# Kernel optimization log

Hardware: AMD Instinct MI355X
Metric: run time of the kernel (lower is better)

Reference implementation:

```python
import jax, jax.numpy as jnp
import numpy as np

N, E, F_IN, HID, H, EDIM, G = 50000, 800000, 64, 32, 4, 4, 1024
NEG = 0.2  # LeakyReLU slope (GATv2Conv default)


def _glorot(key, shape):
    s = jnp.sqrt(6.0 / (shape[0] + shape[-1]))
    return jax.random.uniform(key, shape, minval=-s, maxval=s, dtype=jnp.float32)


def setup_inputs() -> dict:
    key = jax.random.key(0)
    ks = jax.random.split(key, 20)
    d = {}
    d["x"] = jax.random.normal(ks[0], (N, F_IN), dtype=jnp.float32)
    d["edge_index"] = jax.random.randint(ks[1], (2, E), 0, N)
    d["edge_attr"] = jax.random.normal(ks[2], (E, EDIM), dtype=jnp.float32)
    d["batch"] = jnp.sort(jax.random.randint(ks[3], (N,), 0, G))
    dims = [F_IN, HID * H, HID * H]
    i = 4
    for l, din in enumerate(dims, 1):
        d[f"Wl{l}"] = _glorot(ks[i], (din, H * HID)); i += 1
        d[f"bl{l}"] = jnp.zeros((H * HID,), jnp.float32)
        d[f"Wr{l}"] = _glorot(ks[i], (din, H * HID)); i += 1
        d[f"br{l}"] = jnp.zeros((H * HID,), jnp.float32)
        d[f"We{l}"] = _glorot(ks[i], (EDIM, H * HID)); i += 1
        d[f"att{l}"] = _glorot(ks[i], (H, HID)); i += 1
        d[f"bias{l}"] = jnp.zeros((H * HID,), jnp.float32)
    d["Wlin"] = _glorot(ks[i], (H * HID, 1)); i += 1
    d["blin"] = jnp.zeros((1,), jnp.float32)
    return d


def _add_self_loops(edge_index, edge_attr):
    # PyG add_self_loops with fill_value='mean': self-loop edge feature is the
    # mean of incoming-edge features (zeros for isolated targets).
    src0, dst0 = edge_index[0], edge_index[1]
    cnt = jax.ops.segment_sum(jnp.ones((src0.shape[0],), jnp.float32), dst0, num_segments=N)
    loop_attr = jax.ops.segment_sum(edge_attr, dst0, num_segments=N) / jnp.maximum(cnt, 1.0)[:, None]
    ar = jnp.arange(N)
    src = jnp.concatenate([src0, ar])
    dst = jnp.concatenate([dst0, ar])
    ea = jnp.concatenate([edge_attr, loop_attr], axis=0)
    return src, dst, ea


def _gatv2_conv(x, src, dst, ea, Wl, bl, Wr, br, We, att, bias):
    n = x.shape[0]
    xl = (x @ Wl + bl).reshape(n, H, HID)   # source transform (message values)
    xr = (x @ Wr + br).reshape(n, H, HID)   # target transform
    e = jax.nn.leaky_relu(xl[src] + xr[dst] + (ea @ We).reshape(-1, H, HID), NEG)  # [Etot,H,C]
    logit = jnp.einsum('ehc,hc->eh', e, att)
    # segment softmax over destination node (every node has a self-loop)
    m = jax.ops.segment_max(logit, dst, num_segments=n)
    p = jnp.exp(logit - m[dst])
    s = jax.ops.segment_sum(p, dst, num_segments=n)
    alpha = p / (s[dst] + 1e-16)
    out = jax.ops.segment_sum(alpha[:, :, None] * xl[src], dst, num_segments=n)
    return out.reshape(n, H * HID) + bias


def reference(x, edge_index, edge_attr, batch,
              Wl1, bl1, Wr1, br1, We1, att1, bias1,
              Wl2, bl2, Wr2, br2, We2, att2, bias2,
              Wl3, bl3, Wr3, br3, We3, att3, bias3,
              Wlin, blin):
    src, dst, ea = _add_self_loops(edge_index, edge_attr)
    h = jax.nn.relu(_gatv2_conv(x, src, dst, ea, Wl1, bl1, Wr1, br1, We1, att1, bias1))
    h = jax.nn.relu(_gatv2_conv(h, src, dst, ea, Wl2, bl2, Wr2, br2, We2, att2, bias2))
    h = _gatv2_conv(h, src, dst, ea, Wl3, bl3, Wr3, br3, We3, att3, bias3)
    # global mean pool over graphs
    cnt = jax.ops.segment_sum(jnp.ones((N,), jnp.float32), batch, num_segments=G)
    pooled = jax.ops.segment_sum(h, batch, num_segments=G) / jnp.maximum(cnt, 1.0)[:, None]
    # dropout p=0.35 is identity in eval mode
    return pooled @ Wlin + blin
```

## Files before the change

kernel.cpp:

```cpp
#include <hip/hip_runtime.h>
#include <math.h>

#define NN 50000
#define EE 800000
#define FIN 64
#define GG 1024
#define ETOT (EE + NN)
#define PSLOT 16

typedef float v2f __attribute__((ext_vector_type(2)));

__global__ __launch_bounds__(256) void k_init(int* __restrict__ deg, int* __restrict__ fillpos,
    float* __restrict__ psum, int* __restrict__ pcnt) {
  int i = blockIdx.x * 256 + threadIdx.x;
  if (i < NN) { deg[i] = 0; fillpos[i] = 0; }
  if (i < GG * PSLOT) { psum[i] = 0.f; pcnt[i] = 0; }
}

__global__ __launch_bounds__(256) void k_deg(const int* __restrict__ dst, int* __restrict__ deg,
    const int* __restrict__ batch, int* __restrict__ pcnt) {
  int e = blockIdx.x * 256 + threadIdx.x;
  if (e < NN) atomicAdd(&pcnt[(batch[e] << 4) | (e & (PSLOT - 1))], 1);
  if (e >= EE) return;
  atomicAdd(&deg[dst[e]], 1);
}

__global__ __launch_bounds__(256) void k_scan1(const int* __restrict__ deg, int* __restrict__ part) {
  __shared__ int s[256];
  int i = blockIdx.x * 256 + threadIdx.x;
  s[threadIdx.x] = (i < NN) ? deg[i] + 1 : 0;
  __syncthreads();
  for (int st = 128; st > 0; st >>= 1) {
    if (threadIdx.x < st) s[threadIdx.x] += s[threadIdx.x + st];
    __syncthreads();
  }
  if (threadIdx.x == 0) part[blockIdx.x] = s[0];
}

__global__ __launch_bounds__(256) void k_scan2(int* __restrict__ part, int nb, int* __restrict__ offsets) {
  __shared__ int s[256];
  int t = threadIdx.x;
  s[t] = (t < nb) ? part[t] : 0;
  __syncthreads();
  for (int st = 1; st < 256; st <<= 1) {
    int a = (t >= st) ? s[t - st] : 0;
    __syncthreads();
    s[t] += a;
    __syncthreads();
  }
  if (t < nb) part[t] = t ? s[t - 1] : 0;
  if (t == 0) offsets[NN] = ETOT;
}

__global__ __launch_bounds__(256) void k_scan3(const int* __restrict__ deg,
    const int* __restrict__ part, int* __restrict__ offsets) {
  __shared__ int s[256];
  int t = threadIdx.x;
  int i = blockIdx.x * 256 + t;
  int v = (i < NN) ? deg[i] + 1 : 0;
  s[t] = v;
  __syncthreads();
  for (int st = 1; st < 256; st <<= 1) {
    int a = (t >= st) ? s[t - st] : 0;
    __syncthreads();
    s[t] += a;
    __syncthreads();
  }
  if (i < NN) offsets[i] = part[blockIdx.x] + s[t] - v;
}

__global__ __launch_bounds__(256) void k_fill(const int* __restrict__ src,
    const int* __restrict__ dst, const int* __restrict__ offsets,
    const int* __restrict__ deg, int* __restrict__ fillpos,
    int2* __restrict__ pr) {
  int i = blockIdx.x * 256 + threadIdx.x;
  if (i < EE) {
    int d = dst[i];
    int p = offsets[d] + atomicAdd(&fillpos[d], 1);
    pr[p] = make_int2(i, src[i]);
  } else if (i < EE + NN) {
    int n = i - EE;
    int p = offsets[n] + deg[n];
    pr[p] = make_int2(EE + n, n);
  }
}

__global__ __launch_bounds__(256) void k_sort(const int* __restrict__ offsets,
    const int* __restrict__ deg, int2* __restrict__ pr) {
  int n = blockIdx.x * 256 + threadIdx.x;
  if (n >= NN) return;
  int lo = offsets[n], d = deg[n];
  for (int i = lo + 1; i < lo + d; i++) {
    int2 key = pr[i];
    int j = i - 1;
    while (j >= lo && pr[j].x > key.x) {
      pr[j + 1] = pr[j];
      j--;
    }
    pr[j + 1] = key;
  }
}

__global__ __launch_bounds__(256) void k_gather(const int2* __restrict__ pr,
    const float* __restrict__ edge_attr, float4* __restrict__ csr_ea) {
  int p = blockIdx.x * 256 + threadIdx.x;
  if (p >= ETOT) return;
  int eid = pr[p].x;
  if (eid < EE) csr_ea[p] = *(const float4*)(edge_attr + (size_t)eid * 4);
}

__global__ __launch_bounds__(256) void k_selfattr(const int* __restrict__ offsets,
    float4* __restrict__ csr_ea) {
  int wave = threadIdx.x >> 6, lane = threadIdx.x & 63;
  int n = blockIdx.x * 4 + wave;
  if (n >= NN) return;
  int lo = offsets[n], d = offsets[n + 1] - lo - 1;
  float4 s = make_float4(0.f, 0.f, 0.f, 0.f);
  for (int i = lane; i < d; i += 64) {
    float4 v = csr_ea[lo + i];
    s.x += v.x; s.y += v.y; s.z += v.z; s.w += v.w;
  }
  #pragma unroll
  for (int off = 1; off < 64; off <<= 1) {
    s.x += __shfl_xor(s.x, off);
    s.y += __shfl_xor(s.y, off);
    s.z += __shfl_xor(s.z, off);
    s.w += __shfl_xor(s.w, off);
  }
  if (lane == 0) {
    float inv = 1.f / fmaxf((float)d, 1.f);
    csr_ea[lo + d] = make_float4(s.x * inv, s.y * inv, s.z * inv, s.w * inv);
  }
}

__global__ __launch_bounds__(256) void k_gemm(const float* __restrict__ X, int K,
    const float* __restrict__ Wl, const float* __restrict__ bl,
    const float* __restrict__ Wr, const float* __restrict__ br,
    float* __restrict__ xl, float* __restrict__ xr) {
  __shared__ float xsT[128][36];
  int row0 = blockIdx.x * 32;
  int nf4 = 32 * K / 4;
  for (int q = threadIdx.x; q < nf4; q += 256) {
    int r = (q * 4) / K, k0 = (q * 4) % K;
    float4 v = make_float4(0.f, 0.f, 0.f, 0.f);
    int gr = row0 + r;
    if (gr < NN) v = *(const float4*)(X + (size_t)gr * K + k0);
    xsT[k0 + 0][r] = v.x;
    xsT[k0 + 1][r] = v.y;
    xsT[k0 + 2][r] = v.z;
    xsT[k0 + 3][r] = v.w;
  }
  __syncthreads();
  int lane = threadIdx.x & 63, wv = threadIdx.x >> 6;
  int c0 = lane * 4, r0 = wv * 8;
  const float* wbase = (c0 < 128) ? (Wl + c0) : (Wr + c0 - 128);
  v2f acc2[4][4];
  #pragma unroll
  for (int rp = 0; rp < 4; rp++) {
    #pragma unroll
    for (int c = 0; c < 4; c++) acc2[rp][c] = (v2f){0.f, 0.f};
  }
  #pragma unroll 4
  for (int k = 0; k < K; k++) {
    float4 w4 = *(const float4*)(wbase + (size_t)k * 128);
    float4 xa = *(const float4*)&xsT[k][r0];
    float4 xb = *(const float4*)&xsT[k][r0 + 4];
    v2f xp[4] = {{xa.x, xa.y}, {xa.z, xa.w}, {xb.x, xb.y}, {xb.z, xb.w}};
    #pragma unroll
    for (int rp = 0; rp < 4; rp++) {
      acc2[rp][0] += xp[rp] * w4.x;
      acc2[rp][1] += xp[rp] * w4.y;
      acc2[rp][2] += xp[rp] * w4.z;
      acc2[rp][3] += xp[rp] * w4.w;
    }
  }
  float4 b4 = (c0 < 128) ? *(const float4*)(bl + c0) : *(const float4*)(br + c0 - 128);
  float* obase = (c0 < 128) ? (xl + c0) : (xr + c0 - 128);
  #pragma unroll
  for (int rp = 0; rp < 4; rp++) {
    #pragma unroll
    for (int h = 0; h < 2; h++) {
      int gr = row0 + r0 + rp * 2 + h;
      if (gr < NN) {
        float4 o;
        o.x = (h ? acc2[rp][0].y : acc2[rp][0].x) + b4.x;
        o.y = (h ? acc2[rp][1].y : acc2[rp][1].x) + b4.y;
        o.z = (h ? acc2[rp][2].y : acc2[rp][2].x) + b4.z;
        o.w = (h ? acc2[rp][3].y : acc2[rp][3].x) + b4.w;
        *(float4*)(obase + (size_t)gr * 128) = o;
      }
    }
  }
}

__global__ __launch_bounds__(64) void k_attn(
    const float* __restrict__ xl, const float* __restrict__ xr,
    const int* __restrict__ offsets, const int2* __restrict__ pr,
    const float4* __restrict__ csr_ea,
    const float* __restrict__ We, const float* __restrict__ att,
    const float* __restrict__ bias, float* __restrict__ hout, int relu_flag,
    const float* __restrict__ Wlin, const int* __restrict__ batch,
    float* __restrict__ psum) {
  int lane = threadIdx.x & 63;
  int t = blockIdx.x;
  if (t >= NN) return;
  int sub = lane >> 4;
  int cl = lane & 15;
  int ch0 = cl * 8;

  v2f xr2[4], we2[4][4], at2[4];
  {
    float4 a = *(const float4*)(xr + (size_t)t * 128 + ch0);
    float4 b = *(const float4*)(xr + (size_t)t * 128 + ch0 + 4);
    xr2[0] = (v2f){a.x, a.y}; xr2[1] = (v2f){a.z, a.w};
    xr2[2] = (v2f){b.x, b.y}; xr2[3] = (v2f){b.z, b.w};
  }
  #pragma unroll
  for (int k = 0; k < 4; k++) {
    float4 a = *(const float4*)(We + k * 128 + ch0);
    float4 b = *(const float4*)(We + k * 128 + ch0 + 4);
    we2[k][0] = (v2f){a.x, a.y}; we2[k][1] = (v2f){a.z, a.w};
    we2[k][2] = (v2f){b.x, b.y}; we2[k][3] = (v2f){b.z, b.w};
  }
  {
    float4 a = *(const float4*)(att + ch0);
    float4 b = *(const float4*)(att + ch0 + 4);
    at2[0] = (v2f){a.x, a.y}; at2[1] = (v2f){a.z, a.w};
    at2[2] = (v2f){b.x, b.y}; at2[3] = (v2f){b.z, b.w};
  }

  float den = 0.f;
  v2f acc2[4];
  #pragma unroll
  for (int j = 0; j < 4; j++) acc2[j] = (v2f){0.f, 0.f};

  int lo = offsets[t], hi = offsets[t + 1];
  int p = lo + sub;
  int s0 = 0;
  float4 ea0 = make_float4(0.f, 0.f, 0.f, 0.f);
  if (p < hi) { int2 q = pr[p]; s0 = q.y; ea0 = csr_ea[p]; }

  #pragma unroll 1
  for (; p < hi; p += 4) {
    const float* xlb = xl + (size_t)s0 * 128 + ch0;
    float4 xa = *(const float4*)(xlb);
    float4 xb = *(const float4*)(xlb + 4);
    int pn = p + 4;
    int s1 = 0;
    float4 ea1 = make_float4(0.f, 0.f, 0.f, 0.f);
    if (pn < hi) { int2 q = pr[pn]; s1 = q.y; ea1 = csr_ea[pn]; }

    v2f xls2[4] = {{xa.x, xa.y}, {xa.z, xa.w}, {xb.x, xb.y}, {xb.z, xb.w}};
    v2f d2 = (v2f){0.f, 0.f};
    #pragma unroll
    for (int j = 0; j < 4; j++) {
      v2f e2 = xls2[j] + xr2[j];
      e2 += we2[0][j] * ea0.x;
      e2 += we2[1][j] * ea0.y;
      e2 += we2[2][j] * ea0.z;
      e2 += we2[3][j] * ea0.w;
      v2f mx = {fmaxf(e2.x, 0.f), fmaxf(e2.y, 0.f)};
      e2 = e2 * 0.2f + mx * 0.8f;
      d2 += e2 * at2[j];
    }
    float part = d2.x + d2.y;
    part += __shfl_xor(part, 1);
    part += __shfl_xor(part, 2);
    float pe = __expf(part);
    den += pe;
    #pragma unroll
    for (int j = 0; j < 4; j++) acc2[j] += xls2[j] * pe;
    s0 = s1; ea0 = ea1;
  }

  #pragma unroll
  for (int off = 16; off <= 32; off <<= 1) {
    den += __shfl_xor(den, off);
    #pragma unroll
    for (int j = 0; j < 4; j++) {
      v2f o;
      o.x = __shfl_xor(acc2[j].x, off);
      o.y = __shfl_xor(acc2[j].y, off);
      acc2[j] += o;
    }
  }

  if (sub == 0) {
    float inv = 1.f / (den + 1e-16f);
    v2f bs2[4];
    {
      float4 c = *(const float4*)(bias + ch0);
      float4 d = *(const float4*)(bias + ch0 + 4);
      bs2[0] = (v2f){c.x, c.y}; bs2[1] = (v2f){c.z, c.w};
      bs2[2] = (v2f){d.x, d.y}; bs2[3] = (v2f){d.z, d.w};
    }
    v2f o2[4];
    #pragma unroll
    for (int j = 0; j < 4; j++) {
      o2[j] = acc2[j] * inv + bs2[j];
      if (relu_flag) {
        o2[j].x = fmaxf(o2[j].x, 0.f);
        o2[j].y = fmaxf(o2[j].y, 0.f);
      }
    }
    if (psum == nullptr) {
      float* ob = hout + (size_t)t * 128 + ch0;
      *(float4*)(ob) = make_float4(o2[0].x, o2[0].y, o2[1].x, o2[1].y);
      *(float4*)(ob + 4) = make_float4(o2[2].x, o2[2].y, o2[3].x, o2[3].y);
    } else {
      float4 wa = *(const float4*)(Wlin + ch0);
      float4 wb = *(const float4*)(Wlin + ch0 + 4);
      v2f wl2[4] = {{wa.x, wa.y}, {wa.z, wa.w}, {wb.x, wb.y}, {wb.z, wb.w}};
      v2f pd = o2[0] * wl2[0];
      pd += o2[1] * wl2[1];
      pd += o2[2] * wl2[2];
      pd += o2[3] * wl2[3];
      float pv = pd.x + pd.y;
      pv += __shfl_xor(pv, 1);
      pv += __shfl_xor(pv, 2);
      pv += __shfl_xor(pv, 4);
      pv += __shfl_xor(pv, 8);
      if (cl == 0) atomicAdd(&psum[(batch[t] << 4) | (t & (PSLOT - 1))], pv);
    }
  }
}

__global__ __launch_bounds__(256) void k_fin(const float* __restrict__ psum,
    const int* __restrict__ pcnt, const float* __restrict__ blin, float* __restrict__ out) {
  int g = blockIdx.x * 256 + threadIdx.x;
  if (g >= GG) return;
  float s = 0.f;
  int c = 0;
  #pragma unroll
  for (int k = 0; k < PSLOT; k++) {
    s += psum[(g << 4) | k];
    c += pcnt[(g << 4) | k];
  }
  out[g] = s / fmaxf((float)c, 1.f) + blin[0];
}

extern "C" void kernel_launch(void* const* d_in, const int* in_sizes, int n_in,
                              void* d_out, int out_size, void* d_ws, size_t ws_size,
                              hipStream_t stream) {
  const float* x = (const float*)d_in[0];
  const int* ei = (const int*)d_in[1];
  const float* edge_attr = (const float*)d_in[2];
  const int* batch = (const int*)d_in[3];
  const float *Wl[3], *bl[3], *Wr[3], *br[3], *We[3], *att[3], *bias[3];
  for (int l = 0; l < 3; l++) {
    int b = 4 + l * 7;
    Wl[l] = (const float*)d_in[b + 0];
    bl[l] = (const float*)d_in[b + 1];
    Wr[l] = (const float*)d_in[b + 2];
    br[l] = (const float*)d_in[b + 3];
    We[l] = (const float*)d_in[b + 4];
    att[l] = (const float*)d_in[b + 5];
    bias[l] = (const float*)d_in[b + 6];
  }
  const float* Wlin = (const float*)d_in[25];
  const float* blin = (const float*)d_in[26];
  float* out = (float*)d_out;

  const int* src = ei;
  const int* dst = ei + EE;

  char* p = (char*)d_ws;
  size_t used = 0;
  auto carve = [&](size_t bytes) -> void* {
    void* r = p + used;
    used += (bytes + 255) & ~(size_t)255;
    return r;
  };
  int* deg = (int*)carve(NN * sizeof(int));
  int* fillpos = (int*)carve(NN * sizeof(int));
  int* offsets = (int*)carve((NN + 1) * sizeof(int));
  int* part = (int*)carve(256 * sizeof(int));
  int2* pr = (int2*)carve((size_t)ETOT * sizeof(int2));
  float4* csr_ea = (float4*)carve((size_t)ETOT * sizeof(float4));
  float* xl = (float*)carve((size_t)NN * 128 * sizeof(float));
  float* xr = (float*)carve((size_t)NN * 128 * sizeof(float));
  float* hbuf = (float*)carve((size_t)NN * 128 * sizeof(float));
  float* psum = (float*)carve(GG * PSLOT * sizeof(float));
  int* pcnt = (int*)carve(GG * PSLOT * sizeof(int));
  if (used > ws_size) return;

  const int NB = (NN + 255) / 256;

  k_init<<<NB, 256, 0, stream>>>(deg, fillpos, psum, pcnt);
  k_deg<<<(EE + 255) / 256, 256, 0, stream>>>(dst, deg, batch, pcnt);
  k_scan1<<<NB, 256, 0, stream>>>(deg, part);
  k_scan2<<<1, 256, 0, stream>>>(part, NB, offsets);
  k_scan3<<<NB, 256, 0, stream>>>(deg, part, offsets);
  k_fill<<<(EE + NN + 255) / 256, 256, 0, stream>>>(src, dst, offsets, deg, fillpos, pr);
  k_sort<<<NB, 256, 0, stream>>>(offsets, deg, pr);
  k_gather<<<(ETOT + 255) / 256, 256, 0, stream>>>(pr, edge_attr, csr_ea);

  const int GEMM_NB = (NN + 31) / 32;
  const int NODE_NB = (NN + 3) / 4;

  k_selfattr<<<NODE_NB, 256, 0, stream>>>(offsets, csr_ea);

  k_gemm<<<GEMM_NB, 256, 0, stream>>>(x, FIN, Wl[0], bl[0], Wr[0], br[0], xl, xr);
  k_attn<<<NN, 64, 0, stream>>>(xl, xr, offsets, pr, csr_ea, We[0], att[0], bias[0], hbuf, 1,
                                nullptr, nullptr, nullptr);
  k_gemm<<<GEMM_NB, 256, 0, stream>>>(hbuf, 128, Wl[1], bl[1], Wr[1], br[1], xl, xr);
  k_attn<<<NN, 64, 0, stream>>>(xl, xr, offsets, pr, csr_ea, We[1], att[1], bias[1], hbuf, 1,
                                nullptr, nullptr, nullptr);
  k_gemm<<<GEMM_NB, 256, 0, stream>>>(hbuf, 128, Wl[2], bl[2], Wr[2], br[2], xl, xr);
  k_attn<<<NN, 64, 0, stream>>>(xl, xr, offsets, pr, csr_ea, We[2], att[2], bias[2], nullptr, 0,
                                Wlin, batch, psum);

  k_fin<<<(GG + 255) / 256, 256, 0, stream>>>(psum, pcnt, blin, out);
}
```

Baseline: 504.9 us.

## Drop per-segment edge sort, fuse attribute gather into fill, rewrite GEMM without LDS

Removes the per-node insertion sort of CSR entries and the separate edge-attribute gather kernel. Edge attributes are now written directly inside the atomic fill pass. Edge order within each destination segment therefore becomes nondeterministic, which changes floating-point summation order but not the math. The node GEMM also drops its shared-memory transpose and reads X rows directly into registers with a register-blocked v2f accumulation, removing the LDS staging and barrier.

```diff
diff --git a/kernel.cpp b/kernel.cpp
--- a/kernel.cpp
+++ b/kernel.cpp
@@ -9,6 +9,7 @@
 #define PSLOT 16
 
 typedef float v2f __attribute__((ext_vector_type(2)));
+typedef float v4f __attribute__((ext_vector_type(4)));
 
 __global__ __launch_bounds__(256) void k_init(int* __restrict__ deg, int* __restrict__ fillpos,
     float* __restrict__ psum, int* __restrict__ pcnt) {
@@ -72,41 +73,19 @@
 __global__ __launch_bounds__(256) void k_fill(const int* __restrict__ src,
     const int* __restrict__ dst, const int* __restrict__ offsets,
     const int* __restrict__ deg, int* __restrict__ fillpos,
-    int2* __restrict__ pr) {
+    int2* __restrict__ pr, float4* __restrict__ csr_ea,
+    const float* __restrict__ edge_attr) {
   int i = blockIdx.x * 256 + threadIdx.x;
   if (i < EE) {
     int d = dst[i];
     int p = offsets[d] + atomicAdd(&fillpos[d], 1);
     pr[p] = make_int2(i, src[i]);
+    csr_ea[p] = *(const float4*)(edge_attr + (size_t)i * 4);
   } else if (i < EE + NN) {
     int n = i - EE;
     int p = offsets[n] + deg[n];
     pr[p] = make_int2(EE + n, n);
   }
-}
-
-__global__ __launch_bounds__(256) void k_sort(const int* __restrict__ offsets,
-    const int* __restrict__ deg, int2* __restrict__ pr) {
-  int n = blockIdx.x * 256 + threadIdx.x;
-  if (n >= NN) return;
-  int lo = offsets[n], d = deg[n];
-  for (int i = lo + 1; i < lo + d; i++) {
-    int2 key = pr[i];
-    int j = i - 1;
-    while (j >= lo && pr[j].x > key.x) {
-      pr[j + 1] = pr[j];
-      j--;
-    }
-    pr[j + 1] = key;
-  }
-}
-
-__global__ __launch_bounds__(256) void k_gather(const int2* __restrict__ pr,
-    const float* __restrict__ edge_attr, float4* __restrict__ csr_ea) {
-  int p = blockIdx.x * 256 + threadIdx.x;
-  if (p >= ETOT) return;
-  int eid = pr[p].x;
-  if (eid < EE) csr_ea[p] = *(const float4*)(edge_attr + (size_t)eid * 4);
 }
 
 __global__ __launch_bounds__(256) void k_selfattr(const int* __restrict__ offsets,
@@ -137,58 +116,49 @@
     const float* __restrict__ Wl, const float* __restrict__ bl,
     const float* __restrict__ Wr, const float* __restrict__ br,
     float* __restrict__ xl, float* __restrict__ xr) {
-  __shared__ float xsT[128][36];
-  int row0 = blockIdx.x * 32;
-  int nf4 = 32 * K / 4;
-  for (int q = threadIdx.x; q < nf4; q += 256) {
-    int r = (q * 4) / K, k0 = (q * 4) % K;
-    float4 v = make_float4(0.f, 0.f, 0.f, 0.f);
+  int lane = threadIdx.x & 63, wv = threadIdx.x >> 6;
+  int c0 = lane * 4;
+  int row0 = blockIdx.x * 32 + wv * 8;
+  const float* wbase = (c0 < 128) ? (Wl + c0) : (Wr + c0 - 128);
+  const float* xbase[8];
+  #pragma unroll
+  for (int r = 0; r < 8; r++) {
     int gr = row0 + r;
-    if (gr < NN) v = *(const float4*)(X + (size_t)gr * K + k0);
-    xsT[k0 + 0][r] = v.x;
-    xsT[k0 + 1][r] = v.y;
-    xsT[k0 + 2][r] = v.z;
-    xsT[k0 + 3][r] = v.w;
-  }
-  __syncthreads();
-  int lane = threadIdx.x & 63, wv = threadIdx.x >> 6;
-  int c0 = lane * 4, r0 = wv * 8;
-  const float* wbase = (c0 < 128) ? (Wl + c0) : (Wr + c0 - 128);
-  v2f acc2[4][4];
-  #pragma unroll
-  for (int rp = 0; rp < 4; rp++) {
-    #pragma unroll
-    for (int c = 0; c < 4; c++) acc2[rp][c] = (v2f){0.f, 0.f};
-  }
-  #pragma unroll 4
-  for (int k = 0; k < K; k++) {
-    float4 w4 = *(const float4*)(wbase + (size_t)k * 128);
-    float4 xa = *(const float4*)&xsT[k][r0];
-    float4 xb = *(const float4*)&xsT[k][r0 + 4];
-    v2f xp[4] = {{xa.x, xa.y}, {xa.z, xa.w}, {xb.x, xb.y}, {xb.z, xb.w}};
-    #pragma unroll
-    for (int rp = 0; rp < 4; rp++) {
-      acc2[rp][0] += xp[rp] * w4.x;
-      acc2[rp][1] += xp[rp] * w4.y;
-      acc2[rp][2] += xp[rp] * w4.z;
-      acc2[rp][3] += xp[rp] * w4.w;
-    }
-  }
+    xbase[r] = X + (size_t)(gr < NN ? gr : NN - 1) * K;
+  }
+  v2f acc[8][2];
+  #pragma unroll
+  for (int r = 0; r < 8; r++) { acc[r][0] = (v2f){0.f, 0.f}; acc[r][1] = (v2f){0.f, 0.f}; }
+
+  for (int k0 = 0; k0 < K; k0 += 4) {
+    v4f xv[8];
+    #pragma unroll
+    for (int r = 0; r < 8; r++) xv[r] = *(const v4f*)(xbase[r] + k0);
+    v4f w4[4];
+    #pragma unroll
+    for (int kk = 0; kk < 4; kk++) w4[kk] = *(const v4f*)(wbase + (k0 + kk) * 128);
+    #pragma unroll
+    for (int kk = 0; kk < 4; kk++) {
+      v2f wlo = (v2f){w4[kk][0], w4[kk][1]};
+      v2f whi = (v2f){w4[kk][2], w4[kk][3]};
+      #pragma unroll
+      for (int r = 0; r < 8; r++) {
+        float xs = xv[r][kk];
+        acc[r][0] += wlo * xs;
+        acc[r][1] += whi * xs;
+      }
+    }
+  }
+
   float4 b4 = (c0 < 128) ? *(const float4*)(bl + c0) : *(const float4*)(br + c0 - 128);
   float* obase = (c0 < 128) ? (xl + c0) : (xr + c0 - 128);
   #pragma unroll
-  for (int rp = 0; rp < 4; rp++) {
-    #pragma unroll
-    for (int h = 0; h < 2; h++) {
-      int gr = row0 + r0 + rp * 2 + h;
-      if (gr < NN) {
-        float4 o;
-        o.x = (h ? acc2[rp][0].y : acc2[rp][0].x) + b4.x;
-        o.y = (h ? acc2[rp][1].y : acc2[rp][1].x) + b4.y;
-        o.z = (h ? acc2[rp][2].y : acc2[rp][2].x) + b4.z;
-        o.w = (h ? acc2[rp][3].y : acc2[rp][3].x) + b4.w;
-        *(float4*)(obase + (size_t)gr * 128) = o;
-      }
+  for (int r = 0; r < 8; r++) {
+    int gr = row0 + r;
+    if (gr < NN) {
+      float4 o = make_float4(acc[r][0].x + b4.x, acc[r][0].y + b4.y,
+                             acc[r][1].x + b4.z, acc[r][1].y + b4.w);
+      *(float4*)(obase + (size_t)gr * 128) = o;
     }
   }
 }
@@ -391,9 +361,7 @@
   k_scan1<<<NB, 256, 0, stream>>>(deg, part);
   k_scan2<<<1, 256, 0, stream>>>(part, NB, offsets);
   k_scan3<<<NB, 256, 0, stream>>>(deg, part, offsets);
-  k_fill<<<(EE + NN + 255) / 256, 256, 0, stream>>>(src, dst, offsets, deg, fillpos, pr);
-  k_sort<<<NB, 256, 0, stream>>>(offsets, deg, pr);
-  k_gather<<<(ETOT + 255) / 256, 256, 0, stream>>>(pr, edge_attr, csr_ea);
+  k_fill<<<(EE + NN + 255) / 256, 256, 0, stream>>>(src, dst, offsets, deg, fillpos, pr, csr_ea, edge_attr);
 
   const int GEMM_NB = (NN + 31) / 32;
   const int NODE_NB = (NN + 3) / 4;
```

Result: slower. 538.1 us (+6.6%).
